# Performance work log

Measured on AMD Instinct MI355X. Metric: run time of the kernel, lower is better.

## Reference

```python
import jax, jax.numpy as jnp
import numpy as np

B, N, C = 4, 2048, 1024
H = 16
HD = C // H  # 64
THETA = 10000.0


def setup_inputs() -> dict:
    key = jax.random.key(0)
    k1, k2, k3, k4 = jax.random.split(key, 4)
    x = jax.random.normal(k1, (B, N, C), dtype=jnp.float32)
    # Linear-style init scaling to keep activations sane
    w_qkv = jax.random.normal(k2, (3 * C, C), dtype=jnp.float32) * (1.0 / np.sqrt(C))
    w_proj = jax.random.normal(k3, (C, C), dtype=jnp.float32) * (1.0 / np.sqrt(C))
    b_proj = jax.random.normal(k4, (C,), dtype=jnp.float32) * 0.01
    # RoPE frequencies: freqs_cis[n, j] = exp(i * n * theta^(-2j/hd))
    inv_freq = 1.0 / (THETA ** (jnp.arange(0, HD, 2, dtype=jnp.float32) / HD))  # (HD/2,)
    angles = jnp.arange(N, dtype=jnp.float32)[:, None] * inv_freq[None, :]  # (N, HD/2)
    freqs_cos = jnp.cos(angles)
    freqs_sin = jnp.sin(angles)
    return {"x": x, "w_qkv": w_qkv, "w_proj": w_proj, "b_proj": b_proj,
            "freqs_cos": freqs_cos, "freqs_sin": freqs_sin}


def _apply_rope(t, cos, sin):
    # t: (B, N, H, HD) -> complex pairs on last dim
    tr = t.reshape(t.shape[:-1] + (HD // 2, 2))
    a, b = tr[..., 0], tr[..., 1]
    c = cos[None, :, None, :]  # (1, N, 1, HD/2)
    s = sin[None, :, None, :]
    out = jnp.stack([a * c - b * s, a * s + b * c], axis=-1)
    return out.reshape(t.shape)


def reference(x, w_qkv, w_proj, b_proj, freqs_cos, freqs_sin):
    Bx, Nx, Cx = x.shape
    scale = HD ** -0.5
    qkv = jnp.einsum('bnc,dc->bnd', x, w_qkv)  # (B, N, 3C)
    qkv = qkv.reshape(Bx, Nx, 3, H, HD)
    q, k, v = qkv[:, :, 0], qkv[:, :, 1], qkv[:, :, 2]  # (B, N, H, HD)
    q = _apply_rope(q, freqs_cos, freqs_sin)
    k = _apply_rope(k, freqs_cos, freqs_sin)
    # (B, H, N, HD)
    q = q.transpose(0, 2, 1, 3)
    k = k.transpose(0, 2, 1, 3)
    v = v.transpose(0, 2, 1, 3)
    attn = jnp.einsum('bhnd,bhmd->bhnm', q, k) * scale
    attn = jax.nn.softmax(attn, axis=-1)
    out = jnp.einsum('bhnm,bhmd->bhnd', attn, v)  # (B, H, N, HD)
    out = out.transpose(0, 2, 1, 3).reshape(Bx, Nx, Cx)
    return jnp.einsum('bnc,dc->bnd', out, w_proj) + b_proj
```

## Files before the change

### kernel.cpp

```cpp
#include <hip/hip_runtime.h>
#include <hip/hip_bf16.h>
#include <stdint.h>

#define B_  4
#define N_  2048
#define C_  1024
#define H_  16
#define HD_ 64
#define M_  (B_*N_)
#define K3_ (3*C_)

typedef __bf16 bf16;
typedef __bf16 bf16x8 __attribute__((ext_vector_type(8)));
typedef __bf16 bf16x4 __attribute__((ext_vector_type(4)));
typedef float f32x4 __attribute__((ext_vector_type(4)));
typedef float f32x16 __attribute__((ext_vector_type(16)));

#if __has_builtin(__builtin_amdgcn_exp2f)
#define EXP2(x) __builtin_amdgcn_exp2f(x)
#else
#define EXP2(x) exp2f(x)
#endif

__global__ void castk3(const float* __restrict__ a, bf16* __restrict__ oa, int na4,
                       const float* __restrict__ b, bf16* __restrict__ ob, int nb4,
                       const float* __restrict__ c, bf16* __restrict__ oc, int nc4) {
    int total = na4 + nb4 + nc4;
    int stride = gridDim.x * blockDim.x;
    for (int i = blockIdx.x * blockDim.x + threadIdx.x; i < total; i += stride) {
        const float* src; bf16* dst; int j = i;
        if (j < na4)              { src = a; dst = oa; }
        else if ((j -= na4) < nb4){ src = b; dst = ob; }
        else                      { j -= nb4; src = c; dst = oc; }
        float4 v = reinterpret_cast<const float4*>(src)[j];
        bf16x4 o;
        o[0] = (bf16)v.x; o[1] = (bf16)v.y; o[2] = (bf16)v.z; o[3] = (bf16)v.w;
        *reinterpret_cast<bf16x4*>(dst + (size_t)j * 4) = o;
    }
}

__device__ __forceinline__ void gll16(const bf16* g, const bf16* l) {
    __builtin_amdgcn_global_load_lds(
        (const __attribute__((address_space(1))) void*)g,
        (__attribute__((address_space(3))) void*)l, 16, 0, 0);
}

__device__ __forceinline__ uint32_t pkbf(float a, float b) {
    union { bf16 h[2]; uint32_t u; } U;
    U.h[0] = (bf16)a; U.h[1] = (bf16)b;
    return U.u;
}

__device__ __forceinline__ uint32_t pkraw(bf16 a, bf16 b) {
    union { bf16 h[2]; uint32_t u; } U;
    U.h[0] = a; U.h[1] = b;
    return U.u;
}

__device__ __forceinline__ float max3f(float a, float b, float c) {
    float d;
    asm("v_max3_f32 %0, %1, %2, %3" : "=v"(d) : "v"(a), "v"(b), "v"(c));
    return d;
}

template<int MODE>
__global__ __launch_bounds__(256, 4)
void gemm_bt(const bf16* __restrict__ A, const bf16* __restrict__ Bm,
             int Nn, int Kk,
             bf16* __restrict__ qout, bf16* __restrict__ kout, bf16* __restrict__ vout,
             const float* __restrict__ fcos, const float* __restrict__ fsin,
             const float* __restrict__ bias, float* __restrict__ Cout)
{
    __shared__ bf16 a_lds[2][128 * 32];
    __shared__ bf16 b_lds[2][128 * 32];
    const int tid  = threadIdx.x;
    const int lane = tid & 63;
    const int w    = tid >> 6;
    const int wr   = w >> 1, wc = w & 1;
    const int ntile = Nn >> 7;
    const int nwg = gridDim.x, cpx = nwg >> 3;
    const int swz = (blockIdx.x & 7) * cpx + (blockIdx.x >> 3);
    const int bx = swz % ntile, by = swz / ntile;
    const int m0 = by * 128, n0 = bx * 128;

    f32x4 acc[4][4] = {};

    const int c0 = tid, c1 = tid + 256;
    const bf16* ga0 = A  + (size_t)(m0 + (c0 >> 2)) * Kk + (c0 & 3) * 8;
    const bf16* ga1 = A  + (size_t)(m0 + (c1 >> 2)) * Kk + (c1 & 3) * 8;
    const bf16* gb0 = Bm + (size_t)(n0 + (c0 >> 2)) * Kk + (c0 & 3) * 8;
    const bf16* gb1 = Bm + (size_t)(n0 + (c1 >> 2)) * Kk + (c1 & 3) * 8;

    const int rA = lane & 15;
    const int kk = (lane >> 4) * 8;

    gll16(ga0, &a_lds[0][w * 512]);
    gll16(ga1, &a_lds[0][w * 512 + 2048]);
    gll16(gb0, &b_lds[0][w * 512]);
    gll16(gb1, &b_lds[0][w * 512 + 2048]);
    __syncthreads();

    for (int k0 = 0; k0 < Kk; k0 += 32) {
        const int cur = (k0 >> 5) & 1, nxt = cur ^ 1;
        if (k0 + 32 < Kk) {
            gll16(ga0 + k0 + 32, &a_lds[nxt][w * 512]);
            gll16(ga1 + k0 + 32, &a_lds[nxt][w * 512 + 2048]);
            gll16(gb0 + k0 + 32, &b_lds[nxt][w * 512]);
            gll16(gb1 + k0 + 32, &b_lds[nxt][w * 512 + 2048]);
        }

        bf16x8 af[4], bfr[4];
#pragma unroll
        for (int m = 0; m < 4; ++m)
            af[m] = *reinterpret_cast<const bf16x8*>(&a_lds[cur][(wr * 64 + m * 16 + rA) * 32 + kk]);
#pragma unroll
        for (int n = 0; n < 4; ++n)
            bfr[n] = *reinterpret_cast<const bf16x8*>(&b_lds[cur][(wc * 64 + n * 16 + rA) * 32 + kk]);
#pragma unroll
        for (int m = 0; m < 4; ++m)
#pragma unroll
            for (int n = 0; n < 4; ++n)
                acc[m][n] = __builtin_amdgcn_mfma_f32_16x16x32_bf16(af[m], bfr[n], acc[m][n], 0, 0, 0);
        __syncthreads();
    }

    if (MODE == 1) {
#pragma unroll
        for (int n = 0; n < 4; ++n) {
            int cg = n0 + wc * 64 + n * 16 + (lane & 15);
            float bv = bias[cg];
#pragma unroll
            for (int m = 0; m < 4; ++m) {
                int rg = m0 + wr * 64 + m * 16 + (lane >> 4) * 4;
#pragma unroll
                for (int r = 0; r < 4; ++r)
                    Cout[(size_t)(rg + r) * Nn + cg] = acc[m][n][r] + bv;
            }
        }
    } else {
        const int part = n0 >> 10;
#pragma unroll
        for (int n = 0; n < 4; ++n) {
            int cg  = n0 + wc * 64 + n * 16 + (lane & 15);
            int rem = cg & 1023;
            int h   = rem >> 6, hd = rem & 63;
#pragma unroll
            for (int m = 0; m < 4; ++m) {
#pragma unroll
                for (int r = 0; r < 4; ++r) {
                    int rg   = m0 + wr * 64 + m * 16 + (lane >> 4) * 4 + r;
                    int b    = rg >> 11, nrow = rg & 2047;
                    float val = acc[m][n][r];
                    size_t oi = ((size_t)(b * 16 + h) * N_ + nrow) * HD_ + hd;
                    if (part == 2) {
                        vout[oi] = (bf16)val;
                    } else {
                        float p   = __shfl_xor(val, 1);
                        float cth = fcos[nrow * 32 + (hd >> 1)];
                        float sth = fsin[nrow * 32 + (hd >> 1)];
                        float o   = (lane & 1) ? (val * cth + p * sth) : (val * cth - p * sth);
                        if (part == 0) { o *= 0.18033688011112042f; qout[oi] = (bf16)o; }
                        else           { kout[oi] = (bf16)o; }
                    }
                }
            }
        }
    }
}

#define NT_ (N_ / 64)
__global__ __launch_bounds__(256, 2)
void attn_kernel(const bf16* __restrict__ Q, const bf16* __restrict__ Kb,
                 const bf16* __restrict__ Vb, bf16* __restrict__ Ob)
{
    __shared__ bf16 k_lds[2][64 * 64];
    __shared__ bf16 vt_lds[2][64 * 64];
    const int tid = threadIdx.x, lane = tid & 63, w = tid >> 6;
    const int h5  = lane >> 5;
    const int l31 = lane & 31;
    const int nqt = N_ / 128;
    const int cpx = gridDim.x >> 3;
    const int swzb = (blockIdx.x & 7) * cpx + (blockIdx.x >> 3);
    const int bh = swzb / nqt, qt = swzb % nqt;
    const size_t base = (size_t)bh * N_ * HD_;
    const int q0 = qt * 128 + w * 32;

    bf16x8 qf[4];
    {
        const bf16* qp = Q + base + (size_t)(q0 + l31) * HD_ + h5 * 8;
#pragma unroll
        for (int t = 0; t < 4; ++t)
            qf[t] = *reinterpret_cast<const bf16x8*>(qp + t * 16);
    }

    f32x16 oT[2] = {};
    float m_run = 0.0f, l_run = 0.f;

    const int kRowA = tid >> 3;
    const int kColA = ((tid & 7) ^ (kRowA & 7)) * 8;
    const int kRowB = kRowA + 32;
    const int kColB = ((tid & 7) ^ (kRowB & 7)) * 8;
    const bf16* kSrcA = Kb + base + (size_t)kRowA * HD_ + kColA;
    const bf16* kSrcB = Kb + base + (size_t)kRowB * HD_ + kColB;

    const int kp = tid & 31, dc = tid >> 5;
    const bf16* vSrc0 = Vb + base + (size_t)(2 * kp) * HD_ + dc * 8;
    const bf16* vSrc1 = vSrc0 + HD_;

#define STORE_VT(bufidx, va, vb) do {                                              \
        char* vtb = reinterpret_cast<char*>(&vt_lds[0][0]) + (bufidx) * 8192;      \
        _Pragma("unroll")                                                          \
        for (int j = 0; j < 8; ++j) {                                              \
            int byteoff = (dc * 8 + j) * 128 + ((4 * kp) ^ (j << 4));              \
            *reinterpret_cast<uint32_t*>(vtb + byteoff) = pkraw((va)[j], (vb)[j]); \
        }                                                                          \
    } while (0)

    bf16x8 v0 = *reinterpret_cast<const bf16x8*>(vSrc0);
    bf16x8 v1 = *reinterpret_cast<const bf16x8*>(vSrc1);
    gll16(kSrcA, &k_lds[0][w * 512]);
    gll16(kSrcB, &k_lds[0][2048 + w * 512]);
    STORE_VT(0, v0, v1);
    __syncthreads();

    for (int it = 0; it < NT_; ++it) {
        const int cur = it & 1, nxt = cur ^ 1;
        const bool more = (it + 1 < NT_);

        if (more) {
            size_t adv = (size_t)(it + 1) * 64 * HD_;
            v0 = *reinterpret_cast<const bf16x8*>(vSrc0 + adv);
            v1 = *reinterpret_cast<const bf16x8*>(vSrc1 + adv);
            gll16(kSrcA + adv, &k_lds[nxt][w * 512]);
            gll16(kSrcB + adv, &k_lds[nxt][2048 + w * 512]);
        }

        const char* kbase = reinterpret_cast<const char*>(&k_lds[0][0]) + cur * 8192;
        const float negm = -m_run;
        f32x16 st[2];
        __builtin_amdgcn_s_setprio(1);
#pragma unroll
        for (int s = 0; s < 2; ++s) {
            f32x16 acc;
#pragma unroll
            for (int i = 0; i < 16; ++i) acc[i] = negm;
            int row = s * 32 + l31;
#pragma unroll
            for (int t = 0; t < 4; ++t) {
                int cc = (2 * t + h5) ^ (row & 7);
                bf16x8 kf = *reinterpret_cast<const bf16x8*>(kbase + row * 128 + cc * 16);
                acc = __builtin_amdgcn_mfma_f32_32x32x16_bf16(kf, qf[t], acc, 0, 0, 0);
            }
            st[s] = acc;
        }
        __builtin_amdgcn_s_setprio(0);

        float y[8];
#pragma unroll
        for (int i = 0; i < 8; ++i) y[i] = max3f(st[0][i], st[0][i + 8], st[1][i]);
        float z[4];
#pragma unroll
        for (int i = 0; i < 4; ++i) z[i] = max3f(y[i], y[i + 4], st[1][i + 8]);
        float z2 = max3f(z[0], z[1], st[1][12]);
        float z3 = max3f(z[2], z[3], st[1][13]);
        float pm = fmaxf(max3f(z2, z3, st[1][14]), st[1][15]);
        pm = fmaxf(pm, __shfl_xor(pm, 32));
        if (__any(pm > 6.0f)) {
            float d     = fmaxf(pm, 0.0f);
            float alpha = EXP2(-d);
            m_run += d;
            l_run *= alpha;
#pragma unroll
            for (int n = 0; n < 2; ++n)
#pragma unroll
                for (int i = 0; i < 16; ++i) oT[n][i] *= alpha;
#pragma unroll
            for (int s = 0; s < 2; ++s)
#pragma unroll
                for (int i = 0; i < 16; ++i) st[s][i] -= d;
        }
#pragma unroll
        for (int s = 0; s < 2; ++s)
#pragma unroll
            for (int i = 0; i < 16; ++i)
                st[s][i] = EXP2(st[s][i]);
        float t8[8];
#pragma unroll
        for (int i = 0; i < 8; ++i)
            t8[i] = (st[0][i] + st[0][i + 8]) + (st[1][i] + st[1][i + 8]);
#pragma unroll
        for (int i = 0; i < 4; ++i) t8[i] = t8[i] + t8[i + 4];
        float psum = (t8[0] + t8[1]) + (t8[2] + t8[3]);
        psum += __shfl_xor(psum, 32);
        l_run += psum;

        if (more) STORE_VT(nxt, v0, v1);

        const char* vtbase = reinterpret_cast<const char*>(&vt_lds[0][0]) + cur * 8192;
#pragma unroll
        for (int s = 0; s < 2; ++s) {
            uint32_t pk2[4][2];
#pragma unroll
            for (int g = 0; g < 4; ++g) {
                pk2[g][0] = pkbf(st[s][4 * g + 0], st[s][4 * g + 1]);
                pk2[g][1] = pkbf(st[s][4 * g + 2], st[s][4 * g + 3]);
            }
#pragma unroll
            for (int tt = 0; tt < 2; ++tt) {
                const int t = 2 * s + tt;
                uint32_t a0 = pk2[2 * tt][0], b0 = pk2[2 * tt + 1][0];
                uint32_t a1 = pk2[2 * tt][1], b1 = pk2[2 * tt + 1][1];
                asm volatile("v_permlane32_swap_b32 %0, %1" : "+v"(a0), "+v"(b0));
                asm volatile("v_permlane32_swap_b32 %0, %1" : "+v"(a1), "+v"(b1));
                union { uint32_t u[4]; bf16x8 v; } U;
                U.u[0] = a0; U.u[1] = a1; U.u[2] = b0; U.u[3] = b1;
                __builtin_amdgcn_s_setprio(1);
#pragma unroll
                for (int n = 0; n < 2; ++n) {
                    int row = n * 32 + l31;
                    int cc  = (2 * t + h5) ^ (row & 7);
                    bf16x8 vf = *reinterpret_cast<const bf16x8*>(vtbase + row * 128 + cc * 16);
                    oT[n] = __builtin_amdgcn_mfma_f32_32x32x16_bf16(vf, U.v, oT[n], 0, 0, 0);
                }
                __builtin_amdgcn_s_setprio(0);
            }
        }
        __syncthreads();
    }

    const int b = bh >> 4, hh = bh & 15;
    float inv = 1.0f / l_run;
    int q = q0 + l31;
#pragma unroll
    for (int n = 0; n < 2; ++n)
#pragma unroll
        for (int g = 0; g < 4; ++g) {
            int d = n * 32 + 8 * g + 4 * h5;
            bf16x4 o4;
#pragma unroll
            for (int r = 0; r < 4; ++r) o4[r] = (bf16)(oT[n][4 * g + r] * inv);
            *reinterpret_cast<bf16x4*>(Ob + ((size_t)(b * N_ + q)) * C_ + hh * 64 + d) = o4;
        }
#undef STORE_VT
}

extern "C" void kernel_launch(void* const* d_in, const int* in_sizes, int n_in,
                              void* d_out, int out_size, void* d_ws, size_t ws_size,
                              hipStream_t stream) {
    const float* x     = (const float*)d_in[0];
    const float* wqkv  = (const float*)d_in[1];
    const float* wproj = (const float*)d_in[2];
    const float* bproj = (const float*)d_in[3];
    const float* fcos  = (const float*)d_in[4];
    const float* fsin  = (const float*)d_in[5];
    float* out = (float*)d_out;

    bf16* x_bf     = (bf16*)d_ws;
    bf16* wqkv_bf  = x_bf    + (size_t)M_ * C_;
    bf16* wproj_bf = wqkv_bf + (size_t)K3_ * C_;
    bf16* qbuf     = wproj_bf + (size_t)C_ * C_;
    bf16* kbuf     = qbuf  + (size_t)M_ * C_;
    bf16* vbuf     = kbuf  + (size_t)M_ * C_;
    bf16* abuf     = vbuf  + (size_t)M_ * C_;

    castk3<<<2048, 256, 0, stream>>>(x,     x_bf,     M_ * C_ / 4,
                                     wqkv,  wqkv_bf,  K3_ * C_ / 4,
                                     wproj, wproj_bf, C_ * C_ / 4);

    gemm_bt<0><<<64 * 24, 256, 0, stream>>>(x_bf, wqkv_bf, K3_, C_,
                                            qbuf, kbuf, vbuf, fcos, fsin, nullptr, nullptr);
    attn_kernel<<<64 * 16, 256, 0, stream>>>(qbuf, kbuf, vbuf, abuf);
    gemm_bt<1><<<64 * 8, 256, 0, stream>>>(abuf, wproj_bf, C_, C_,
                                           nullptr, nullptr, nullptr, nullptr, nullptr, bproj, out);
}
```

Before: 245.5 us.

## Use 256x256 tiled 8-wave GEMM with swizzled LDS for QKV projection

```diff
diff --git a/kernel.cpp b/kernel.cpp
--- a/kernel.cpp
+++ b/kernel.cpp
@@ -9,6 +9,7 @@
 #define HD_ 64
 #define M_  (B_*N_)
 #define K3_ (3*C_)
+#define NKT_ 16
 
 typedef __bf16 bf16;
 typedef __bf16 bf16x8 __attribute__((ext_vector_type(8)));
@@ -63,12 +64,128 @@
     return d;
 }
 
+__global__ __launch_bounds__(512, 2)
+void gemm256(const bf16* __restrict__ A, const bf16* __restrict__ Bm,
+             int Nn, int Kk,
+             bf16* __restrict__ qout, bf16* __restrict__ kout, bf16* __restrict__ vout,
+             const float* __restrict__ fcos, const float* __restrict__ fsin)
+{
+    __shared__ bf16 Ab[2][2][128 * 64];
+    __shared__ bf16 Bb[2][2][128 * 64];
+    const int tid = threadIdx.x, lane = tid & 63, w = tid >> 6;
+    const int wm = w >> 2, wn = w & 3;
+    const int ntile = Nn >> 8;
+    const int cpx = gridDim.x >> 3;
+    const int swz = (blockIdx.x & 7) * cpx + (blockIdx.x >> 3);
+    const int bx = swz % ntile, by = swz / ntile;
+    const int m0 = by * 256, n0 = bx * 256;
+
+    f32x4 acc[8][4] = {};
+
+    const int ci0 = tid, ci1 = tid + 512;
+    const int sr0 = ci0 >> 3, sc0 = ((ci0 & 7) ^ (sr0 & 7)) * 8;
+    const int sr1 = ci1 >> 3, sc1 = ((ci1 & 7) ^ (sr1 & 7)) * 8;
+    const bf16* sA00 = A  + (size_t)(m0 + sr0) * Kk + sc0;
+    const bf16* sA01 = A  + (size_t)(m0 + sr1) * Kk + sc1;
+    const bf16* sA10 = A  + (size_t)(m0 + 128 + sr0) * Kk + sc0;
+    const bf16* sA11 = A  + (size_t)(m0 + 128 + sr1) * Kk + sc1;
+    const bf16* sB00 = Bm + (size_t)(n0 + sr0) * Kk + sc0;
+    const bf16* sB01 = Bm + (size_t)(n0 + sr1) * Kk + sc1;
+    const bf16* sB10 = Bm + (size_t)(n0 + 128 + sr0) * Kk + sc0;
+    const bf16* sB11 = Bm + (size_t)(n0 + 128 + sr1) * Kk + sc1;
+    const int d0 = w * 512;
+    const int d1 = w * 512 + 4096;
+
+    const int rl = lane & 15, hi = lane >> 4;
+    const int x7 = rl & 7;
+    const int h3 = (hi ^ (x7 & 3)) * 16;
+    const int k4 = (x7 & 4) * 16;
+    const int lb0 = rl * 128 + h3 + k4;
+    const int lb1 = rl * 128 + h3 + (64 - k4);
+
+    gll16(sA00, &Ab[0][0][d0]); gll16(sA01, &Ab[0][0][d1]);
+    gll16(sA10, &Ab[0][1][d0]); gll16(sA11, &Ab[0][1][d1]);
+    gll16(sB00, &Bb[0][0][d0]); gll16(sB01, &Bb[0][0][d1]);
+    gll16(sB10, &Bb[0][1][d0]); gll16(sB11, &Bb[0][1][d1]);
+
+    for (int kt = 0; kt < NKT_; ++kt) {
+        const int slot = kt & 1, nslot = slot ^ 1;
+        const char* aB = reinterpret_cast<const char*>(&Ab[slot][wm][0]);
+        const char* bB = reinterpret_cast<const char*>(&Bb[slot][wn >> 1][0]) + (wn & 1) * 8192;
+        const bool more = (kt + 1 < NKT_);
+        const int adv = (kt + 1) * 64;
+#pragma unroll
+        for (int q = 0; q < 4; ++q) {
+            if (more) {
+                if (q == 0) { gll16(sA00 + adv, &Ab[nslot][0][d0]); gll16(sA01 + adv, &Ab[nslot][0][d1]); }
+                if (q == 1) { gll16(sA10 + adv, &Ab[nslot][1][d0]); gll16(sA11 + adv, &Ab[nslot][1][d1]); }
+                if (q == 2) { gll16(sB00 + adv, &Bb[nslot][0][d0]); gll16(sB01 + adv, &Bb[nslot][0][d1]); }
+                if (q == 3) { gll16(sB10 + adv, &Bb[nslot][1][d0]); gll16(sB11 + adv, &Bb[nslot][1][d1]); }
+            }
+            if (q == 0) {
+                if (more) asm volatile("s_waitcnt vmcnt(2)" ::: "memory");
+                else      asm volatile("s_waitcnt vmcnt(0)" ::: "memory");
+            }
+            __builtin_amdgcn_s_barrier();
+
+            bf16x8 af[2][2], bfr[4][2];
+#pragma unroll
+            for (int mf = 0; mf < 2; ++mf) {
+                af[mf][0] = *reinterpret_cast<const bf16x8*>(aB + (q * 32 + mf * 16) * 128 + lb0);
+                af[mf][1] = *reinterpret_cast<const bf16x8*>(aB + (q * 32 + mf * 16) * 128 + lb1);
+            }
+#pragma unroll
+            for (int nf = 0; nf < 4; ++nf) {
+                bfr[nf][0] = *reinterpret_cast<const bf16x8*>(bB + nf * 2048 + lb0);
+                bfr[nf][1] = *reinterpret_cast<const bf16x8*>(bB + nf * 2048 + lb1);
+            }
+            __builtin_amdgcn_s_setprio(1);
+#pragma unroll
+            for (int ks = 0; ks < 2; ++ks)
+#pragma unroll
+                for (int mf = 0; mf < 2; ++mf)
+#pragma unroll
+                    for (int nf = 0; nf < 4; ++nf)
+                        acc[q * 2 + mf][nf] = __builtin_amdgcn_mfma_f32_16x16x32_bf16(
+                            af[mf][ks], bfr[nf][ks], acc[q * 2 + mf][nf], 0, 0, 0);
+            __builtin_amdgcn_s_setprio(0);
+            __builtin_amdgcn_s_barrier();
+        }
+    }
+
+    const int part = n0 >> 10;
+#pragma unroll
+    for (int j = 0; j < 4; ++j) {
+        int cg  = n0 + wn * 64 + j * 16 + (lane & 15);
+        int rem = cg & 1023;
+        int h   = rem >> 6, hd = rem & 63;
+#pragma unroll
+        for (int i = 0; i < 8; ++i) {
+#pragma unroll
+            for (int r = 0; r < 4; ++r) {
+                int rg = m0 + wm * 128 + i * 16 + (lane >> 4) * 4 + r;
+                int b  = rg >> 11, nrow = rg & 2047;
+                float val = acc[i][j][r];
+                size_t oi = ((size_t)(b * 16 + h) * N_ + nrow) * HD_ + hd;
+                if (part == 2) {
+                    vout[oi] = (bf16)val;
+                } else {
+                    float p   = __shfl_xor(val, 1);
+                    float cth = fcos[nrow * 32 + (hd >> 1)];
+                    float sth = fsin[nrow * 32 + (hd >> 1)];
+                    float o   = (lane & 1) ? (val * cth + p * sth) : (val * cth - p * sth);
+                    if (part == 0) { o *= 0.18033688011112042f; qout[oi] = (bf16)o; }
+                    else           { kout[oi] = (bf16)o; }
+                }
+            }
+        }
+    }
+}
+
 template<int MODE>
 __global__ __launch_bounds__(256, 4)
 void gemm_bt(const bf16* __restrict__ A, const bf16* __restrict__ Bm,
              int Nn, int Kk,
-             bf16* __restrict__ qout, bf16* __restrict__ kout, bf16* __restrict__ vout,
-             const float* __restrict__ fcos, const float* __restrict__ fsin,
              const float* __restrict__ bias, float* __restrict__ Cout)
 {
     __shared__ bf16 a_lds[2][128 * 32];
@@ -108,7 +225,6 @@
             gll16(gb0 + k0 + 32, &b_lds[nxt][w * 512]);
             gll16(gb1 + k0 + 32, &b_lds[nxt][w * 512 + 2048]);
         }
-
         bf16x8 af[4], bfr[4];
 #pragma unroll
         for (int m = 0; m < 4; ++m)
@@ -124,46 +240,16 @@
         __syncthreads();
     }
 
-    if (MODE == 1) {
-#pragma unroll
-        for (int n = 0; n < 4; ++n) {
-            int cg = n0 + wc * 64 + n * 16 + (lane & 15);
-            float bv = bias[cg];
-#pragma unroll
-            for (int m = 0; m < 4; ++m) {
-                int rg = m0 + wr * 64 + m * 16 + (lane >> 4) * 4;
-#pragma unroll
-                for (int r = 0; r < 4; ++r)
-                    Cout[(size_t)(rg + r) * Nn + cg] = acc[m][n][r] + bv;
-            }
-        }
-    } else {
-        const int part = n0 >> 10;
-#pragma unroll
-        for (int n = 0; n < 4; ++n) {
-            int cg  = n0 + wc * 64 + n * 16 + (lane & 15);
-            int rem = cg & 1023;
-            int h   = rem >> 6, hd = rem & 63;
-#pragma unroll
-            for (int m = 0; m < 4; ++m) {
-#pragma unroll
-                for (int r = 0; r < 4; ++r) {
-                    int rg   = m0 + wr * 64 + m * 16 + (lane >> 4) * 4 + r;
-                    int b    = rg >> 11, nrow = rg & 2047;
-                    float val = acc[m][n][r];
-                    size_t oi = ((size_t)(b * 16 + h) * N_ + nrow) * HD_ + hd;
-                    if (part == 2) {
-                        vout[oi] = (bf16)val;
-                    } else {
-                        float p   = __shfl_xor(val, 1);
-                        float cth = fcos[nrow * 32 + (hd >> 1)];
-                        float sth = fsin[nrow * 32 + (hd >> 1)];
-                        float o   = (lane & 1) ? (val * cth + p * sth) : (val * cth - p * sth);
-                        if (part == 0) { o *= 0.18033688011112042f; qout[oi] = (bf16)o; }
-                        else           { kout[oi] = (bf16)o; }
-                    }
-                }
-            }
+#pragma unroll
+    for (int n = 0; n < 4; ++n) {
+        int cg = n0 + wc * 64 + n * 16 + (lane & 15);
+        float bv = bias[cg];
+#pragma unroll
+        for (int m = 0; m < 4; ++m) {
+            int rg = m0 + wr * 64 + m * 16 + (lane >> 4) * 4;
+#pragma unroll
+            for (int r = 0; r < 4; ++r)
+                Cout[(size_t)(rg + r) * Nn + cg] = acc[m][n][r] + bv;
         }
     }
 }
@@ -238,7 +324,6 @@
         const char* kbase = reinterpret_cast<const char*>(&k_lds[0][0]) + cur * 8192;
         const float negm = -m_run;
         f32x16 st[2];
-        __builtin_amdgcn_s_setprio(1);
 #pragma unroll
         for (int s = 0; s < 2; ++s) {
             f32x16 acc;
@@ -253,7 +338,6 @@
             }
             st[s] = acc;
         }
-        __builtin_amdgcn_s_setprio(0);
 
         float y[8];
 #pragma unroll
@@ -314,7 +398,6 @@
                 asm volatile("v_permlane32_swap_b32 %0, %1" : "+v"(a1), "+v"(b1));
                 union { uint32_t u[4]; bf16x8 v; } U;
                 U.u[0] = a0; U.u[1] = a1; U.u[2] = b0; U.u[3] = b1;
-                __builtin_amdgcn_s_setprio(1);
 #pragma unroll
                 for (int n = 0; n < 2; ++n) {
                     int row = n * 32 + l31;
@@ -322,7 +405,6 @@
                     bf16x8 vf = *reinterpret_cast<const bf16x8*>(vtbase + row * 128 + cc * 16);
                     oT[n] = __builtin_amdgcn_mfma_f32_32x32x16_bf16(vf, U.v, oT[n], 0, 0, 0);
                 }
-                __builtin_amdgcn_s_setprio(0);
             }
         }
         __syncthreads();
@@ -367,9 +449,8 @@
                                      wqkv,  wqkv_bf,  K3_ * C_ / 4,
                                      wproj, wproj_bf, C_ * C_ / 4);
 
-    gemm_bt<0><<<64 * 24, 256, 0, stream>>>(x_bf, wqkv_bf, K3_, C_,
-                                            qbuf, kbuf, vbuf, fcos, fsin, nullptr, nullptr);
+    gemm256<<<32 * 12, 512, 0, stream>>>(x_bf, wqkv_bf, K3_, C_,
+                                         qbuf, kbuf, vbuf, fcos, fsin);
     attn_kernel<<<64 * 16, 256, 0, stream>>>(qbuf, kbuf, vbuf, abuf);
-    gemm_bt<1><<<64 * 8, 256, 0, stream>>>(abuf, wproj_bf, C_, C_,
-                                           nullptr, nullptr, nullptr, nullptr, nullptr, bproj, out);
-}
+    gemm_bt<1><<<64 * 8, 256, 0, stream>>>(abuf, wproj_bf, C_, C_, bproj, out);
+}
```

New measurement: 294.0 us. +19.8%, slower.
